# Optimization experiments

Measured on AMD Instinct MI355X. Metric: run time of the kernel, lower is better.

The kernel has to match this reference:

```python
import jax, jax.numpy as jnp
import numpy as np

VOCAB_SIZE = 62  # string.ascii_letters + string.digits
HIDDEN = 1024
STATE = int(HIDDEN * 4.0)  # state_size_mult=4.0
B, L = 2, 2048


def setup_inputs() -> dict:
    key = jax.random.key(0)
    ks = jax.random.split(key, 6)
    g = lambda k, shape, scale: (jax.random.normal(k, shape, jnp.float32) * scale)
    return {
        "tokens": jax.random.randint(ks[0], (B, L), 0, VOCAB_SIZE),
        "embed_w": g(ks[1], (VOCAB_SIZE, HIDDEN), 1.0),
        "norm_w": jnp.ones((HIDDEN,), jnp.float32),
        "in_w": g(ks[2], (HIDDEN, 4 * STATE), HIDDEN ** -0.5),
        "in_b": jnp.zeros((4 * STATE,), jnp.float32),
        "out_w": g(ks[3], (STATE, HIDDEN), STATE ** -0.5),
        "out_b": jnp.zeros((HIDDEN,), jnp.float32),
        "head_w": g(ks[4], (HIDDEN, VOCAB_SIZE), HIDDEN ** -0.5),
        "head_b": jnp.zeros((VOCAB_SIZE,), jnp.float32),
    }


def _rmsnorm(x, w, eps=1e-6):
    var = jnp.mean(x * x, axis=-1, keepdims=True)
    return x * jax.lax.rsqrt(var + eps) * w


def reference(tokens, embed_w, norm_w, in_w, in_b, out_w, out_b, head_w, head_b):
    # embedding lookup: [B, L, H]
    x = embed_w[tokens]
    res = x
    xn = _rmsnorm(x, norm_w)
    # single fused projection to (x_inner, a, b, c), each [B, L, STATE]
    proj = xn @ in_w + in_b
    xg, a_l, b_l, c_l = jnp.split(proj, 4, axis=-1)
    a = jax.nn.sigmoid(a_l)            # forget gate in (0,1)
    bx = jax.nn.sigmoid(b_l) * xg      # input contribution b_t * x_t
    # linear recurrence h_t = a_t * h_{t-1} + b_t * x_t via associative scan
    def comb(e1, e2):
        a1, h1 = e1
        a2, h2 = e2
        return a1 * a2, a2 * h1 + h2
    _, h = jax.lax.associative_scan(comb, (a, bx), axis=1)
    y = jax.nn.sigmoid(c_l) * h        # output gate c_t * h_t
    out = y @ out_w + out_b + res      # project back to hidden + residual
    return out @ head_w + head_b       # vocab logits [B, L, 62]
```

## Files before the change

### kernel.cpp

```cpp
#include <hip/hip_runtime.h>
#include <math.h>

#define HID   1024
#define STT   4096
#define MTOK  4096
#define LSEQ  2048
#define NCHUNK 64
#define CHUNK  32
#define VOCAB  62

typedef __attribute__((ext_vector_type(8))) short short8v;
typedef __attribute__((ext_vector_type(4))) float float4v;

typedef const __attribute__((address_space(1))) void* gptr_t;
typedef __attribute__((address_space(3))) void* lptr_t;

__device__ __forceinline__ float sigmoidf_(float x) {
    return 1.0f / (1.0f + __expf(-x));
}
__device__ __forceinline__ unsigned short f2bf(float f) {
    unsigned int u = __float_as_uint(f);
    unsigned int r = (u + 0x7fffu + ((u >> 16) & 1u)) >> 16;
    return (unsigned short)r;
}
__device__ __forceinline__ float bf2f(unsigned short b) {
    return __uint_as_float(((unsigned int)b) << 16);
}

__global__ __launch_bounds__(256) void cast_transpose_kernel(
    const float* __restrict__ src, unsigned short* __restrict__ dst, int R, int C)
{
    __shared__ float tile[32][33];
    int c0 = blockIdx.x * 32, r0 = blockIdx.y * 32;
    int t = threadIdx.x;
    int r = t >> 3, c4 = (t & 7) << 2;
    float4 v = *(const float4*)(src + (size_t)(r0 + r) * C + c0 + c4);
    tile[r][c4 + 0] = v.x; tile[r][c4 + 1] = v.y;
    tile[r][c4 + 2] = v.z; tile[r][c4 + 3] = v.w;
    __syncthreads();
    int oc = t >> 3;
    int orr = (t & 7) << 2;
    ushort4 o;
    o.x = f2bf(tile[orr + 0][oc]); o.y = f2bf(tile[orr + 1][oc]);
    o.z = f2bf(tile[orr + 2][oc]); o.w = f2bf(tile[orr + 3][oc]);
    *(ushort4*)(dst + (size_t)(c0 + oc) * R + r0 + orr) = o;
}

__global__ __launch_bounds__(256) void embed_norm_kernel(
    const int* __restrict__ tokens, const float* __restrict__ embed_w,
    const float* __restrict__ norm_w, unsigned short* __restrict__ xn)
{
    int m = blockIdx.x;
    int t = threadIdx.x;
    int tok = tokens[m];
    float4 x = ((const float4*)(embed_w + (size_t)tok * HID))[t];
    float ss = x.x * x.x + x.y * x.y + x.z * x.z + x.w * x.w;
    for (int off = 32; off > 0; off >>= 1) ss += __shfl_down(ss, off);
    __shared__ float wsum[4];
    if ((t & 63) == 0) wsum[t >> 6] = ss;
    __syncthreads();
    float tot = wsum[0] + wsum[1] + wsum[2] + wsum[3];
    float scale = rsqrtf(tot / (float)HID + 1e-6f);
    float4 w4 = ((const float4*)norm_w)[t];
    ushort4 o;
    o.x = f2bf(x.x * scale * w4.x); o.y = f2bf(x.y * scale * w4.y);
    o.z = f2bf(x.z * scale * w4.z); o.w = f2bf(x.w * scale * w4.w);
    *(ushort4*)(xn + (size_t)m * HID + (t << 2)) = o;
}

__global__ __launch_bounds__(512, 2) void gemm_in_mfma(
    const unsigned short* __restrict__ A, const unsigned short* __restrict__ B,
    const float* __restrict__ bias,
    unsigned short* __restrict__ a_out, unsigned short* __restrict__ bx_out,
    unsigned short* __restrict__ c_out)
{
    extern __shared__ unsigned short lds[];
    int tid = threadIdx.x;
    int wid = tid >> 6, lane = tid & 63;
    int wg = blockIdx.x;
    int xcd = wg & 7, loc = wg >> 3;
    int by = ((xcd >> 1) << 2) + (loc & 3);
    int bx = ((xcd & 1) << 5) + (loc >> 2);
    int m0 = by * 256, s0 = bx * 64;
    int wm = wid >> 2, wn = wid & 3;
    int lr = lane & 15, lk = lane >> 4;

    int cb0 = wid * 64, cb1 = 512 + wid * 64;
    int p0 = cb0 + lane, p1 = cb1 + lane;
    int row0 = p0 >> 2, ks0 = (p0 & 3) ^ ((row0 >> 1) & 3);
    int row1 = p1 >> 2, ks1 = (p1 & 3) ^ ((row1 >> 1) & 3);
    int arow0 = m0 + row0, arow1 = m0 + row1;
    int brow0 = ((row0 >> 6) << 12) + s0 + (row0 & 63);
    int brow1 = ((row1 >> 6) << 12) + s0 + (row1 & 63);

#define SHALF(grow0, grow1, b, which, kt, kk) do {                               \
    unsigned short* _d = lds + (b) * 32768 + (which) * 16384 + (kk) * 8192;      \
    __builtin_amdgcn_global_load_lds(                                            \
        (gptr_t)(const void*)(((which) ? B : A) + (size_t)(grow0) * 1024 +       \
                              (kt) * 64 + (kk) * 32 + ks0 * 8),                  \
        (lptr_t)(void*)(_d + (size_t)cb0 * 8), 16, 0, 0);                        \
    __builtin_amdgcn_global_load_lds(                                            \
        (gptr_t)(const void*)(((which) ? B : A) + (size_t)(grow1) * 1024 +       \
                              (kt) * 64 + (kk) * 32 + ks1 * 8),                  \
        (lptr_t)(void*)(_d + (size_t)cb1 * 8), 16, 0, 0);                        \
} while (0)

    int ksw = lk ^ ((lr >> 1) & 3);

#define RD_A(b, kk, mf) \
    (*(const short8v*)&lds[(b) * 32768 + (kk) * 8192 + \
        (((wm * 128 + (mf) * 16 + lr) << 2) + ksw) * 8])
#define RD_B(b, kk, nf) \
    (*(const short8v*)&lds[(b) * 32768 + 16384 + (kk) * 8192 + \
        ((((nf) * 64 + wn * 16 + lr) << 2) + ksw) * 8])

#define MFMA8x2(AF, B0, B1, n0i, n1i) do {                                       \
    __builtin_amdgcn_s_setprio(1);                                               \
    _Pragma("unroll")                                                            \
    for (int mf = 0; mf < 8; mf++) {                                             \
        acc[mf][n0i] = __builtin_amdgcn_mfma_f32_16x16x32_bf16(                  \
            (AF)[mf], (B0), acc[mf][n0i], 0, 0, 0);                              \
        acc[mf][n1i] = __builtin_amdgcn_mfma_f32_16x16x32_bf16(                  \
            (AF)[mf], (B1), acc[mf][n1i], 0, 0, 0);                              \
    }                                                                            \
    __builtin_amdgcn_s_setprio(0);                                               \
} while (0)

#define BAR_IN()  do { __builtin_amdgcn_s_barrier();                              \
    asm volatile("s_waitcnt lgkmcnt(0)" ::: "memory");                           \
    __builtin_amdgcn_sched_barrier(0); } while (0)
#define BAR_OUT() do { asm volatile("" ::: "memory");                             \
    __builtin_amdgcn_s_barrier(); } while (0)

    float4v acc[8][4];
    float4v z = {0.f, 0.f, 0.f, 0.f};
    #pragma unroll
    for (int i = 0; i < 8; i++)
        #pragma unroll
        for (int j = 0; j < 4; j++) acc[i][j] = z;

    SHALF(arow0, arow1, 0, 0, 0, 0); SHALF(brow0, brow1, 0, 1, 0, 0);
    SHALF(arow0, arow1, 0, 0, 0, 1); SHALF(brow0, brow1, 0, 1, 0, 1);
    asm volatile("s_waitcnt vmcnt(0)" ::: "memory");
    __builtin_amdgcn_s_barrier();

    short8v af[8], bf0, bf1;

    for (int kt = 0; kt < 16; ++kt) {
        int cur = kt & 1, nxt = cur ^ 1;
        int ktn = kt < 15 ? kt + 1 : 15;
        #pragma unroll
        for (int mf = 0; mf < 8; mf++) af[mf] = RD_A(cur, 0, mf);
        bf0 = RD_B(cur, 0, 0); bf1 = RD_B(cur, 0, 1);
        asm volatile("s_waitcnt vmcnt(4)" ::: "memory");
        SHALF(arow0, arow1, nxt, 0, ktn, 0);
        BAR_IN();
        MFMA8x2(af, bf0, bf1, 0, 1);
        BAR_OUT();
        bf0 = RD_B(cur, 0, 2); bf1 = RD_B(cur, 0, 3);
        SHALF(brow0, brow1, nxt, 1, ktn, 0);
        BAR_IN();
        MFMA8x2(af, bf0, bf1, 2, 3);
        BAR_OUT();
        #pragma unroll
        for (int mf = 0; mf < 8; mf++) af[mf] = RD_A(cur, 1, mf);
        bf0 = RD_B(cur, 1, 0); bf1 = RD_B(cur, 1, 1);
        asm volatile("s_waitcnt vmcnt(4)" ::: "memory");
        SHALF(arow0, arow1, nxt, 0, ktn, 1);
        BAR_IN();
        MFMA8x2(af, bf0, bf1, 0, 1);
        BAR_OUT();
        bf0 = RD_B(cur, 1, 2); bf1 = RD_B(cur, 1, 3);
        SHALF(brow0, brow1, nxt, 1, ktn, 1);
        BAR_IN();
        MFMA8x2(af, bf0, bf1, 2, 3);
        BAR_OUT();
    }

    int s = s0 + wn * 16 + lr;
    float b_xg = bias[s];
    float b_a  = bias[4096 + s];
    float b_b  = bias[8192 + s];
    float b_c  = bias[12288 + s];
    int rbase = lk << 2;
    #pragma unroll
    for (int mf = 0; mf < 8; mf++)
        #pragma unroll
        for (int q = 0; q < 4; q++) {
            int m = m0 + wm * 128 + mf * 16 + rbase + q;
            size_t idx = (size_t)m * STT + s;
            float xg = acc[mf][0][q] + b_xg;
            float a  = sigmoidf_(acc[mf][1][q] + b_a);
            float bxv = sigmoidf_(acc[mf][2][q] + b_b) * xg;
            float c  = sigmoidf_(acc[mf][3][q] + b_c);
            a_out[idx]  = f2bf(a);
            bx_out[idx] = f2bf(bxv);
            c_out[idx]  = f2bf(c);
        }
#undef SHALF
#undef RD_A
#undef RD_B
#undef MFMA8x2
#undef BAR_IN
#undef BAR_OUT
}

__global__ __launch_bounds__(256, 3) void gemm_out_mfma(
    const unsigned short* __restrict__ A, const unsigned short* __restrict__ B,
    const float* __restrict__ out_b, const int* __restrict__ tokens,
    const float* __restrict__ embed_w, float* __restrict__ Cout)
{
    extern __shared__ unsigned short lds[];
    int tid = threadIdx.x;
    int wid = tid >> 6, lane = tid & 63;
    int wg = blockIdx.x;
    int swz = (wg & 7) * 32 + (wg >> 3);
    int bx = swz & 7;
    int by = swz >> 3;
    int m0 = by * 128, n0 = bx * 128;
    int wm = wid >> 1, wn = wid & 1;
    int lr = lane & 15, lk = lane >> 4;

    auto stage = [&](int b, int kt) {
        unsigned short* As = lds + b * 8192;
        unsigned short* Bs = As + 4096;
        #pragma unroll
        for (int i = 0; i < 2; i++) {
            int cb = i * 256 + wid * 64;
            int p = cb + lane;
            int row = p >> 2;
            int ks = (p & 3) ^ ((row >> 1) & 3);
            __builtin_amdgcn_global_load_lds(
                (gptr_t)(const void*)(A + (size_t)(m0 + row) * 4096 + kt + ks * 8),
                (lptr_t)(void*)(As + (size_t)cb * 8), 16, 0, 0);
            __builtin_amdgcn_global_load_lds(
                (gptr_t)(const void*)(B + (size_t)(n0 + row) * 4096 + kt + ks * 8),
                (lptr_t)(void*)(Bs + (size_t)cb * 8), 16, 0, 0);
        }
    };

    float4v acc[4][4];
    float4v z = {0.f, 0.f, 0.f, 0.f};
    #pragma unroll
    for (int i = 0; i < 4; i++)
        #pragma unroll
        for (int j = 0; j < 4; j++) acc[i][j] = z;

    const int nt = 4096 / 32;
    stage(0, 0); stage(1, 32);

    int ksw = lk ^ ((lr >> 1) & 3);
    int aoff = lr * 4 + ksw;

    for (int t = 0; t < nt; ++t) {
        if (t + 2 < nt) stage((t + 2) % 3, (t + 2) * 32);
        if (t + 2 < nt)      asm volatile("s_waitcnt vmcnt(8)" ::: "memory");
        else if (t + 1 < nt) asm volatile("s_waitcnt vmcnt(4)" ::: "memory");
        else                 asm volatile("s_waitcnt vmcnt(0)" ::: "memory");
        __builtin_amdgcn_s_barrier();
        asm volatile("" ::: "memory");
        const unsigned short* As = lds + (t % 3) * 8192;
        const unsigned short* Bs = As + 4096;
        short8v af[4], bfr[4];
        #pragma unroll
        for (int f = 0; f < 4; f++) {
            af[f]  = *(const short8v*)&As[((wm * 64 + f * 16) * 4 + aoff) * 8];
            bfr[f] = *(const short8v*)&Bs[((wn * 64 + f * 16) * 4 + aoff) * 8];
        }
        __builtin_amdgcn_s_setprio(1);
        #pragma unroll
        for (int mf = 0; mf < 4; mf++)
            #pragma unroll
            for (int nf = 0; nf < 4; nf++)
                acc[mf][nf] = __builtin_amdgcn_mfma_f32_16x16x32_bf16(
                    af[mf], bfr[nf], acc[mf][nf], 0, 0, 0);
        __builtin_amdgcn_s_setprio(0);
        asm volatile("" ::: "memory");
        __builtin_amdgcn_s_barrier();
    }

    int rbase = lk << 2;
    #pragma unroll
    for (int mf = 0; mf < 4; mf++) {
        #pragma unroll
        for (int q = 0; q < 4; q++) {
            int m = m0 + wm * 64 + mf * 16 + rbase + q;
            int tok = tokens[m];
            #pragma unroll
            for (int nf = 0; nf < 4; nf++) {
                int n = n0 + wn * 64 + nf * 16 + lr;
                float v = acc[mf][nf][q] + out_b[n] + embed_w[(size_t)tok * HID + n];
                Cout[(size_t)m * HID + n] = v;
            }
        }
    }
}

__global__ __launch_bounds__(256) void scan_phase1(
    const unsigned short* __restrict__ a_buf, const unsigned short* __restrict__ bx_buf,
    float* __restrict__ chunkA, float* __restrict__ chunkH)
{
    int bid = blockIdx.x;
    int sg = bid & 3, q = (bid >> 2) & 63, b = bid >> 8;
    int s0 = sg * 1024 + threadIdx.x * 4;
    size_t base = (size_t)(b * LSEQ + q * CHUNK) * STT + s0;
    const unsigned short* ap = a_buf + base;
    const unsigned short* bp = bx_buf + base;
    float Aa[4] = {1.f, 1.f, 1.f, 1.f}, Hh[4] = {0.f, 0.f, 0.f, 0.f};
    for (int t = 0; t < CHUNK; t++) {
        ushort4 Av = *(const ushort4*)ap;
        ushort4 Bv = *(const ushort4*)bp;
        const unsigned short* avp = (const unsigned short*)&Av;
        const unsigned short* bvp = (const unsigned short*)&Bv;
        #pragma unroll
        for (int j = 0; j < 4; j++) {
            float a = bf2f(avp[j]);
            Hh[j] = fmaf(a, Hh[j], bf2f(bvp[j]));
            Aa[j] *= a;
        }
        ap += STT; bp += STT;
    }
    #pragma unroll
    for (int j = 0; j < 4; j++) {
        int ch = b * STT + s0 + j;
        chunkA[ch * NCHUNK + q] = Aa[j];
        chunkH[ch * NCHUNK + q] = Hh[j];
    }
}

__global__ __launch_bounds__(256) void scan_phase2(
    const float* __restrict__ chunkA, const float* __restrict__ chunkH,
    float* __restrict__ carry)
{
    int ch = blockIdx.x * 256 + threadIdx.x;
    float c = 0.f;
    for (int q = 0; q < NCHUNK; q++) {
        carry[ch * NCHUNK + q] = c;
        c = fmaf(chunkA[ch * NCHUNK + q], c, chunkH[ch * NCHUNK + q]);
    }
}

__global__ __launch_bounds__(256) void scan_phase3(
    const unsigned short* __restrict__ a_buf, const unsigned short* __restrict__ bx_buf,
    const unsigned short* __restrict__ c_buf, const float* __restrict__ carry,
    unsigned short* __restrict__ y)
{
    int bid = blockIdx.x;
    int sg = bid & 3, q = (bid >> 2) & 63, b = bid >> 8;
    int s0 = sg * 1024 + threadIdx.x * 4;
    float h[4];
    #pragma unroll
    for (int j = 0; j < 4; j++)
        h[j] = carry[(b * STT + s0 + j) * NCHUNK + q];
    size_t base = (size_t)(b * LSEQ + q * CHUNK) * STT + s0;
    const unsigned short* ap = a_buf + base;
    const unsigned short* bp = bx_buf + base;
    const unsigned short* cp = c_buf + base;
    unsigned short* yp = y + base;
    for (int t = 0; t < CHUNK; t++) {
        ushort4 Av = *(const ushort4*)ap;
        ushort4 Bv = *(const ushort4*)bp;
        ushort4 Cv = *(const ushort4*)cp;
        const unsigned short* avp = (const unsigned short*)&Av;
        const unsigned short* bvp = (const unsigned short*)&Bv;
        const unsigned short* cvp = (const unsigned short*)&Cv;
        ushort4 o;
        unsigned short* op = (unsigned short*)&o;
        #pragma unroll
        for (int j = 0; j < 4; j++) {
            h[j] = fmaf(bf2f(avp[j]), h[j], bf2f(bvp[j]));
            op[j] = f2bf(bf2f(cvp[j]) * h[j]);
        }
        *(ushort4*)yp = o;
        ap += STT; bp += STT; cp += STT; yp += STT;
    }
}

__global__ __launch_bounds__(256) void head_kernel(
    const float* __restrict__ out, const float* __restrict__ head_w,
    const float* __restrict__ head_b, float* __restrict__ logits)
{
    __shared__ float row[HID];
    __shared__ float part[4][64];
    int m = blockIdx.x;
    int t = threadIdx.x;
    ((float4*)row)[t] = ((const float4*)(out + (size_t)m * HID))[t];
    __syncthreads();
    int v = t & 63, ks = t >> 6;
    float s = 0.f;
    if (v < VOCAB) {
        const float* wcol = head_w + (size_t)(ks * 256) * VOCAB + v;
        const float* rb = row + ks * 256;
        #pragma unroll 4
        for (int k = 0; k < 256; k++)
            s = fmaf(rb[k], wcol[(size_t)k * VOCAB], s);
    }
    part[ks][v] = s;
    __syncthreads();
    if (t < VOCAB)
        logits[(size_t)m * VOCAB + t] =
            part[0][t] + part[1][t] + part[2][t] + part[3][t] + head_b[t];
}

extern "C" void kernel_launch(void* const* d_in, const int* in_sizes, int n_in,
                              void* d_out, int out_size, void* d_ws, size_t ws_size,
                              hipStream_t stream) {
    const int*   tokens  = (const int*)d_in[0];
    const float* embed_w = (const float*)d_in[1];
    const float* norm_w  = (const float*)d_in[2];
    const float* in_w    = (const float*)d_in[3];
    const float* in_b    = (const float*)d_in[4];
    const float* out_w   = (const float*)d_in[5];
    const float* out_b   = (const float*)d_in[6];
    const float* head_w  = (const float*)d_in[7];
    const float* head_b  = (const float*)d_in[8];
    float* logits = (float*)d_out;

    char* w = (char*)d_ws;
    unsigned short* a_buf  = (unsigned short*)w;
    unsigned short* bx_buf = (unsigned short*)(w + 33554432);
    unsigned short* c_buf  = (unsigned short*)(w + 67108864);
    unsigned short* y      = (unsigned short*)(w + 134217728);
    unsigned short* in_wT  = (unsigned short*)(w + 167772160);
    float*          outbuf = (float*)(w + 167772160);
    unsigned short* xn     = (unsigned short*)(w + 201326592);
    unsigned short* out_wT = (unsigned short*)(w + 201326592);
    float* chunkA = (float*)(w + 209715200);
    float* chunkH = chunkA + 8192 * NCHUNK;
    float* carry  = chunkH + 8192 * NCHUNK;

    hipLaunchKernelGGL(cast_transpose_kernel, dim3(16384 / 32, 1024 / 32), dim3(256), 0, stream,
                       in_w, in_wT, 1024, 16384);
    hipLaunchKernelGGL(embed_norm_kernel, dim3(MTOK), dim3(256), 0, stream,
                       tokens, embed_w, norm_w, xn);
    hipLaunchKernelGGL(gemm_in_mfma, dim3(1024), dim3(512), 131072, stream,
                       xn, in_wT, in_b, a_buf, bx_buf, c_buf);
    hipLaunchKernelGGL(scan_phase1, dim3(512), dim3(256), 0, stream,
                       a_buf, bx_buf, chunkA, chunkH);
    hipLaunchKernelGGL(scan_phase2, dim3(32), dim3(256), 0, stream,
                       chunkA, chunkH, carry);
    hipLaunchKernelGGL(scan_phase3, dim3(512), dim3(256), 0, stream,
                       a_buf, bx_buf, c_buf, carry, y);
    hipLaunchKernelGGL(cast_transpose_kernel, dim3(1024 / 32, 4096 / 32), dim3(256), 0, stream,
                       out_w, out_wT, 4096, 1024);
    hipLaunchKernelGGL(gemm_out_mfma, dim3(256), dim3(256), 49152, stream,
                       y, out_wT, out_b, tokens, embed_w, outbuf);
    hipLaunchKernelGGL(head_kernel, dim3(MTOK), dim3(256), 0, stream,
                       outbuf, head_w, head_b, logits);
}
```

Measured before the change: 312.0 us.

## Fold output projection and head into one precomputed weight product

Uses associativity to precompute W2 = out_w @ head_w (4096x62, bf16) and per-token embedding@head tables. The large 4096x1024x4096 output GEMM and the head kernel become a narrow 4096x64x4096 GEMM, split-K across 8 slices, plus a small reduce. This removes most of the out-projection FLOPs and the fp32 intermediate traffic. In exchange it adds weight-product kernels on every call, and rounding the fused weight to bf16 changes numerics.

```diff
diff --git a/kernel.cpp b/kernel.cpp
--- a/kernel.cpp
+++ b/kernel.cpp
@@ -68,6 +68,43 @@
     *(ushort4*)(xn + (size_t)m * HID + (t << 2)) = o;
 }
 
+__global__ __launch_bounds__(256) void w2t_kernel(
+    const float* __restrict__ out_w, const float* __restrict__ head_w,
+    unsigned short* __restrict__ W2T)
+{
+    int k = blockIdx.x * 4 + (threadIdx.x >> 6);
+    int n = threadIdx.x & 63;
+    float acc = 0.f;
+    const float* wr = out_w + (size_t)k * HID;
+    for (int j = 0; j < HID; j += 4) {
+        float4 wv = *(const float4*)(wr + j);
+        if (n < VOCAB) {
+            acc = fmaf(wv.x, head_w[(size_t)(j + 0) * VOCAB + n], acc);
+            acc = fmaf(wv.y, head_w[(size_t)(j + 1) * VOCAB + n], acc);
+            acc = fmaf(wv.z, head_w[(size_t)(j + 2) * VOCAB + n], acc);
+            acc = fmaf(wv.w, head_w[(size_t)(j + 3) * VOCAB + n], acc);
+        }
+    }
+    W2T[(size_t)n * STT + k] = f2bf(acc);
+}
+
+__global__ __launch_bounds__(64) void ehead_kernel(
+    const float* __restrict__ embed_w, const float* __restrict__ out_b,
+    const float* __restrict__ head_w, const float* __restrict__ head_b,
+    float* __restrict__ E_head)
+{
+    int t = blockIdx.x;
+    int n = threadIdx.x;
+    const float* src = (t < VOCAB) ? (embed_w + (size_t)t * HID) : out_b;
+    float acc = 0.f;
+    if (n < VOCAB) {
+        for (int j = 0; j < HID; j++)
+            acc = fmaf(src[j], head_w[(size_t)j * VOCAB + n], acc);
+        if (t == VOCAB) acc += head_b[n];
+    }
+    E_head[t * 64 + n] = acc;
+}
+
 __global__ __launch_bounds__(512, 2) void gemm_in_mfma(
     const unsigned short* __restrict__ A, const unsigned short* __restrict__ B,
     const float* __restrict__ bias,
@@ -205,24 +242,22 @@
 #undef BAR_OUT
 }
 
-__global__ __launch_bounds__(256, 3) void gemm_out_mfma(
-    const unsigned short* __restrict__ A, const unsigned short* __restrict__ B,
-    const float* __restrict__ out_b, const int* __restrict__ tokens,
-    const float* __restrict__ embed_w, float* __restrict__ Cout)
+__global__ __launch_bounds__(256, 3) void logits_gemm(
+    const unsigned short* __restrict__ Y, const unsigned short* __restrict__ W2T,
+    float* __restrict__ part)
 {
     extern __shared__ unsigned short lds[];
     int tid = threadIdx.x;
     int wid = tid >> 6, lane = tid & 63;
     int wg = blockIdx.x;
-    int swz = (wg & 7) * 32 + (wg >> 3);
-    int bx = swz & 7;
-    int by = swz >> 3;
-    int m0 = by * 128, n0 = bx * 128;
+    int m0 = (wg & 31) * 128;
+    int slice = wg >> 5;
+    int ks0 = slice * 512;
     int wm = wid >> 1, wn = wid & 1;
     int lr = lane & 15, lk = lane >> 4;
 
     auto stage = [&](int b, int kt) {
-        unsigned short* As = lds + b * 8192;
+        unsigned short* As = lds + b * 6144;
         unsigned short* Bs = As + 4096;
         #pragma unroll
         for (int i = 0; i < 2; i++) {
@@ -231,69 +266,86 @@
             int row = p >> 2;
             int ks = (p & 3) ^ ((row >> 1) & 3);
             __builtin_amdgcn_global_load_lds(
-                (gptr_t)(const void*)(A + (size_t)(m0 + row) * 4096 + kt + ks * 8),
+                (gptr_t)(const void*)(Y + (size_t)(m0 + row) * STT + kt + ks * 8),
                 (lptr_t)(void*)(As + (size_t)cb * 8), 16, 0, 0);
+        }
+        {
+            int cb = wid * 64;
+            int p = cb + lane;
+            int row = p >> 2;
+            int ks = (p & 3) ^ ((row >> 1) & 3);
             __builtin_amdgcn_global_load_lds(
-                (gptr_t)(const void*)(B + (size_t)(n0 + row) * 4096 + kt + ks * 8),
+                (gptr_t)(const void*)(W2T + (size_t)row * STT + kt + ks * 8),
                 (lptr_t)(void*)(Bs + (size_t)cb * 8), 16, 0, 0);
         }
     };
 
-    float4v acc[4][4];
+    float4v acc[4][2];
     float4v z = {0.f, 0.f, 0.f, 0.f};
     #pragma unroll
-    for (int i = 0; i < 4; i++)
-        #pragma unroll
-        for (int j = 0; j < 4; j++) acc[i][j] = z;
-
-    const int nt = 4096 / 32;
-    stage(0, 0); stage(1, 32);
+    for (int i = 0; i < 4; i++) { acc[i][0] = z; acc[i][1] = z; }
+
+    const int nt = 16;
+    stage(0, ks0); stage(1, ks0 + 32);
 
     int ksw = lk ^ ((lr >> 1) & 3);
-    int aoff = lr * 4 + ksw;
 
     for (int t = 0; t < nt; ++t) {
-        if (t + 2 < nt) stage((t + 2) % 3, (t + 2) * 32);
-        if (t + 2 < nt)      asm volatile("s_waitcnt vmcnt(8)" ::: "memory");
-        else if (t + 1 < nt) asm volatile("s_waitcnt vmcnt(4)" ::: "memory");
+        if (t + 2 < nt) stage((t + 2) % 3, ks0 + (t + 2) * 32);
+        if (t + 2 < nt)      asm volatile("s_waitcnt vmcnt(6)" ::: "memory");
+        else if (t + 1 < nt) asm volatile("s_waitcnt vmcnt(3)" ::: "memory");
         else                 asm volatile("s_waitcnt vmcnt(0)" ::: "memory");
         __builtin_amdgcn_s_barrier();
         asm volatile("" ::: "memory");
-        const unsigned short* As = lds + (t % 3) * 8192;
+        const unsigned short* As = lds + (t % 3) * 6144;
         const unsigned short* Bs = As + 4096;
-        short8v af[4], bfr[4];
-        #pragma unroll
-        for (int f = 0; f < 4; f++) {
-            af[f]  = *(const short8v*)&As[((wm * 64 + f * 16) * 4 + aoff) * 8];
-            bfr[f] = *(const short8v*)&Bs[((wn * 64 + f * 16) * 4 + aoff) * 8];
-        }
+        short8v af[4], bfr[2];
+        #pragma unroll
+        for (int f = 0; f < 4; f++)
+            af[f] = *(const short8v*)&As[(((wm * 64 + f * 16 + lr) << 2) + ksw) * 8];
+        #pragma unroll
+        for (int g = 0; g < 2; g++)
+            bfr[g] = *(const short8v*)&Bs[(((wn * 32 + g * 16 + lr) << 2) + ksw) * 8];
         __builtin_amdgcn_s_setprio(1);
         #pragma unroll
-        for (int mf = 0; mf < 4; mf++)
+        for (int f = 0; f < 4; f++)
             #pragma unroll
-            for (int nf = 0; nf < 4; nf++)
-                acc[mf][nf] = __builtin_amdgcn_mfma_f32_16x16x32_bf16(
-                    af[mf], bfr[nf], acc[mf][nf], 0, 0, 0);
+            for (int g = 0; g < 2; g++)
+                acc[f][g] = __builtin_amdgcn_mfma_f32_16x16x32_bf16(
+                    af[f], bfr[g], acc[f][g], 0, 0, 0);
         __builtin_amdgcn_s_setprio(0);
         asm volatile("" ::: "memory");
         __builtin_amdgcn_s_barrier();
     }
 
+    float* pb = part + (size_t)slice * MTOK * 64;
     int rbase = lk << 2;
     #pragma unroll
-    for (int mf = 0; mf < 4; mf++) {
-        #pragma unroll
-        for (int q = 0; q < 4; q++) {
-            int m = m0 + wm * 64 + mf * 16 + rbase + q;
-            int tok = tokens[m];
+    for (int f = 0; f < 4; f++)
+        #pragma unroll
+        for (int g = 0; g < 2; g++) {
+            int n = wn * 32 + g * 16 + lr;
             #pragma unroll
-            for (int nf = 0; nf < 4; nf++) {
-                int n = n0 + wn * 64 + nf * 16 + lr;
-                float v = acc[mf][nf][q] + out_b[n] + embed_w[(size_t)tok * HID + n];
-                Cout[(size_t)m * HID + n] = v;
+            for (int q = 0; q < 4; q++) {
+                int m = m0 + wm * 64 + f * 16 + rbase + q;
+                pb[(size_t)m * 64 + n] = acc[f][g][q];
             }
         }
-    }
+}
+
+__global__ __launch_bounds__(64) void logits_reduce(
+    const float* __restrict__ part, const float* __restrict__ E_head,
+    const int* __restrict__ tokens, float* __restrict__ logits)
+{
+    int m = blockIdx.x;
+    int n = threadIdx.x;
+    if (n >= VOCAB) return;
+    int tok = tokens[m];
+    float s = E_head[tok * 64 + n] + E_head[VOCAB * 64 + n];
+    #pragma unroll
+    for (int sl = 0; sl < 8; sl++)
+        s += part[(size_t)sl * MTOK * 64 + (size_t)m * 64 + n];
+    logits[(size_t)m * VOCAB + n] = s;
 }
 
 __global__ __launch_bounds__(256) void scan_phase1(
@@ -376,32 +428,6 @@
     }
 }
 
-__global__ __launch_bounds__(256) void head_kernel(
-    const float* __restrict__ out, const float* __restrict__ head_w,
-    const float* __restrict__ head_b, float* __restrict__ logits)
-{
-    __shared__ float row[HID];
-    __shared__ float part[4][64];
-    int m = blockIdx.x;
-    int t = threadIdx.x;
-    ((float4*)row)[t] = ((const float4*)(out + (size_t)m * HID))[t];
-    __syncthreads();
-    int v = t & 63, ks = t >> 6;
-    float s = 0.f;
-    if (v < VOCAB) {
-        const float* wcol = head_w + (size_t)(ks * 256) * VOCAB + v;
-        const float* rb = row + ks * 256;
-        #pragma unroll 4
-        for (int k = 0; k < 256; k++)
-            s = fmaf(rb[k], wcol[(size_t)k * VOCAB], s);
-    }
-    part[ks][v] = s;
-    __syncthreads();
-    if (t < VOCAB)
-        logits[(size_t)m * VOCAB + t] =
-            part[0][t] + part[1][t] + part[2][t] + part[3][t] + head_b[t];
-}
-
 extern "C" void kernel_launch(void* const* d_in, const int* in_sizes, int n_in,
                               void* d_out, int out_size, void* d_ws, size_t ws_size,
                               hipStream_t stream) {
@@ -420,11 +446,12 @@
     unsigned short* a_buf  = (unsigned short*)w;
     unsigned short* bx_buf = (unsigned short*)(w + 33554432);
     unsigned short* c_buf  = (unsigned short*)(w + 67108864);
+    unsigned short* W2T    = (unsigned short*)(w + 100663296);
+    float*          E_head = (float*)(w + 101711872);
+    float*          part   = (float*)(w + 102760448);
     unsigned short* y      = (unsigned short*)(w + 134217728);
     unsigned short* in_wT  = (unsigned short*)(w + 167772160);
-    float*          outbuf = (float*)(w + 167772160);
     unsigned short* xn     = (unsigned short*)(w + 201326592);
-    unsigned short* out_wT = (unsigned short*)(w + 201326592);
     float* chunkA = (float*)(w + 209715200);
     float* chunkH = chunkA + 8192 * NCHUNK;
     float* carry  = chunkH + 8192 * NCHUNK;
@@ -433,6 +460,10 @@
                        in_w, in_wT, 1024, 16384);
     hipLaunchKernelGGL(embed_norm_kernel, dim3(MTOK), dim3(256), 0, stream,
                        tokens, embed_w, norm_w, xn);
+    hipLaunchKernelGGL(w2t_kernel, dim3(1024), dim3(256), 0, stream,
+                       out_w, head_w, W2T);
+    hipLaunchKernelGGL(ehead_kernel, dim3(VOCAB + 1), dim3(64), 0, stream,
+                       embed_w, out_b, head_w, head_b, E_head);
     hipLaunchKernelGGL(gemm_in_mfma, dim3(1024), dim3(512), 131072, stream,
                        xn, in_wT, in_b, a_buf, bx_buf, c_buf);
     hipLaunchKernelGGL(scan_phase1, dim3(512), dim3(256), 0, stream,
@@ -441,10 +472,8 @@
                        chunkA, chunkH, carry);
     hipLaunchKernelGGL(scan_phase3, dim3(512), dim3(256), 0, stream,
                        a_buf, bx_buf, c_buf, carry, y);
-    hipLaunchKernelGGL(cast_transpose_kernel, dim3(1024 / 32, 4096 / 32), dim3(256), 0, stream,
-                       out_w, out_wT, 4096, 1024);
-    hipLaunchKernelGGL(gemm_out_mfma, dim3(256), dim3(256), 49152, stream,
-                       y, out_wT, out_b, tokens, embed_w, outbuf);
-    hipLaunchKernelGGL(head_kernel, dim3(MTOK), dim3(256), 0, stream,
-                       outbuf, head_w, head_b, logits);
-}
+    hipLaunchKernelGGL(logits_gemm, dim3(256), dim3(256), 36864, stream,
+                       y, W2T, part);
+    hipLaunchKernelGGL(logits_reduce, dim3(MTOK), dim3(64), 0, stream,
+                       part, E_head, tokens, logits);
+}
```

Result: slower. 353.4 us (+13.3%).
